# Kernel tuning notes

Hardware: AMD Instinct MI355X
Metric: run time of the kernel (lower is better)

The kernel has to match this reference:

```python
import jax, jax.numpy as jnp
import numpy as np

D_MODEL = 512
D_STATE = 64
SEQ_LEN = 8192
BATCH = 8
LN_EPS = 1e-3  # keras LayerNormalization default epsilon
DELTA_MIN = 0.001
DELTA_MAX = 0.8 * (2.0 / D_STATE)  # default when use_hippo_init=True


def setup_inputs() -> dict:
    key = jax.random.key(0)
    ks = jax.random.split(key, 10)
    x = jax.random.normal(ks[0], (BATCH, SEQ_LEN, D_MODEL), dtype=jnp.float32)
    # Dense layers: glorot-uniform-ish init via scaled normal for simplicity
    def dense_w(k, fan_in, fan_out):
        lim = np.sqrt(6.0 / (fan_in + fan_out))
        return jax.random.uniform(k, (fan_in, fan_out), minval=-lim, maxval=lim, dtype=jnp.float32)
    W_in = dense_w(ks[1], D_MODEL, D_MODEL)
    b_in = jnp.zeros((D_MODEL,), jnp.float32)
    W_xs = dense_w(ks[2], D_MODEL, D_STATE)
    # HiPPO-LegS log init: A_log = log(n+1)
    A_log = jnp.log(jnp.arange(1, D_STATE + 1, dtype=jnp.float32))
    log_delta = jax.random.uniform(ks[3], (D_STATE,), minval=np.log(DELTA_MIN), maxval=np.log(DELTA_MAX), dtype=jnp.float32)
    B = jnp.ones((D_STATE,), jnp.float32)
    C = jax.random.normal(ks[4], (D_STATE,), dtype=jnp.float32)  # stddev=1.0
    D = jnp.ones((D_MODEL,), jnp.float32)
    W_so = dense_w(ks[5], D_STATE, D_MODEL)
    W_out = dense_w(ks[6], D_MODEL, D_MODEL)
    b_out = jnp.zeros((D_MODEL,), jnp.float32)
    ln_gamma = jnp.ones((D_MODEL,), jnp.float32)
    ln_beta = jnp.zeros((D_MODEL,), jnp.float32)
    return {
        "x": x, "ln_gamma": ln_gamma, "ln_beta": ln_beta,
        "W_in": W_in, "b_in": b_in, "W_xs": W_xs,
        "A_log": A_log, "log_delta": log_delta, "B": B, "C": C, "D": D,
        "W_so": W_so, "W_out": W_out, "b_out": b_out,
    }


def reference(x, ln_gamma, ln_beta, W_in, b_in, W_xs, A_log, log_delta, B, C, D, W_so, W_out, b_out):
    Bsz, L, dm = x.shape
    n_fft = 1 << int(np.ceil(np.log2(2 * L - 1)))
    residual = x
    # LayerNorm over last axis (keras default)
    mu = jnp.mean(x, axis=-1, keepdims=True)
    var = jnp.mean(jnp.square(x - mu), axis=-1, keepdims=True)
    xn = (x - mu) * jax.lax.rsqrt(var + LN_EPS) * ln_gamma + ln_beta
    z = xn @ W_in + b_in                       # (B, L, d_model)
    x_state = z @ W_xs                          # (B, L, d_state)
    # Diagonal SSM discretization (bilinear/Tustin)
    A = -jnp.exp(A_log)
    delta = jax.nn.softplus(log_delta)
    dA2 = delta * A / 2.0
    A_bar = (1.0 + dA2) / (1.0 - dA2)           # (d_state,)
    B_bar = delta / (1.0 - dA2) * B             # (d_state,)
    t = jnp.arange(L, dtype=jnp.float32)
    kernel = jnp.power(A_bar[None, :], t[:, None]) * B_bar[None, :]  # (L, d_state)
    # FFT convolution along time
    u_t = jnp.transpose(x_state, (0, 2, 1))     # (B, d_state, L)
    k_t = kernel.T                              # (d_state, L)
    u_f = jnp.fft.rfft(u_t, n=n_fft, axis=-1)
    k_f = jnp.fft.rfft(k_t, n=n_fft, axis=-1)
    y = jnp.fft.irfft(u_f * k_f[None, :, :], n=n_fft, axis=-1)[:, :, :L]
    y_state = jnp.transpose(y, (0, 2, 1))       # (B, L, d_state)
    y_state = y_state * C[None, None, :]
    y = y_state @ W_so                          # (B, L, d_model)
    y = y + D * z
    y = y @ W_out + b_out
    return y + residual
```

## Files before the change

### kernel.cpp

```cpp
#include <hip/hip_runtime.h>
#include <hip/hip_bf16.h>
#include <cstddef>
#include <cstdint>

#define DM 512
#define DS 64
#define L_SEQ 8192
#define NB 8
#define M_ROWS (NB * L_SEQ)
#define LN_EPS 1e-3f
#define NCHUNK 256
#define LCH 32

typedef __attribute__((ext_vector_type(8))) short short8;
typedef __attribute__((ext_vector_type(4))) float f32x4;
using bf16 = __hip_bfloat16;
using ushort_t = unsigned short;

__device__ __forceinline__ unsigned short f2bf(float f) {
    bf16 h = __float2bfloat16(f);
    return *reinterpret_cast<unsigned short*>(&h);
}

__device__ __forceinline__ int swzcol(int row, int col) {
    return (col & ~63) | (((((col >> 3) & 7) ^ (row & 7))) << 3) | (col & 7);
}

__device__ __forceinline__ size_t pkidx(int k, int n, int Kd32) {
    int n16 = n >> 4, fr = n & 15, kt = k >> 5, fq = (k >> 3) & 3, e = k & 7;
    return (((size_t)(n16 * Kd32 + kt) * 64 + fq * 16 + fr) << 3) + e;
}

__device__ __forceinline__ void gload_lds16(const void* g, void* l) {
    __builtin_amdgcn_global_load_lds(
        (const __attribute__((address_space(1))) void*)g,
        (__attribute__((address_space(3))) void*)l, 16, 0, 0);
}

template<int N> __device__ __forceinline__ void wait_vm() {
    static_assert(N == 0 || N == 2, "");
    if constexpr (N == 0) asm volatile("s_waitcnt vmcnt(0)" ::: "memory");
    else                  asm volatile("s_waitcnt vmcnt(2)" ::: "memory");
}

__device__ __forceinline__ void block_barrier() {
    asm volatile("" ::: "memory");
    __builtin_amdgcn_s_barrier();
    asm volatile("" ::: "memory");
}

__global__ __launch_bounds__(256) void prep(const float* __restrict__ W_so,
                                            const float* __restrict__ W_out,
                                            const float* __restrict__ W_in,
                                            const float* __restrict__ W_xs,
                                            const float* __restrict__ b_in,
                                            const float* __restrict__ b_out,
                                            const float* __restrict__ Dv,
                                            float* __restrict__ sWc2,
                                            float* __restrict__ sWc1,
                                            float* __restrict__ bc1,
                                            float* __restrict__ sWc3,
                                            float* __restrict__ bc2)
{
    int i = blockIdx.x * 256 + threadIdx.x;
    if (i < 32768) {
        int s = i >> 9, j = i & 511;
        float a = 0.f;
        for (int c = 0; c < 512; ++c) a += W_so[s * 512 + c] * W_out[c * 512 + j];
        sWc2[i] = a;
    } else if (i < 65536) {
        int idx = i - 32768; int k = idx >> 6, n = idx & 63;
        float a = 0.f;
        for (int c = 0; c < 512; ++c) a += W_in[k * 512 + c] * W_xs[c * 64 + n];
        sWc1[idx] = a;
    } else if (i < 65600) {
        int n = i - 65536;
        float a = 0.f;
        for (int c = 0; c < 512; ++c) a += b_in[c] * W_xs[c * 64 + n];
        bc1[n] = a;
    } else if (i < 327744) {
        int idx = i - 65600; int k = idx >> 9, j = idx & 511;
        float a = 0.f;
        for (int c = 0; c < 512; ++c) a += W_in[k * 512 + c] * Dv[c] * W_out[c * 512 + j];
        sWc3[idx] = a;
    } else if (i < 328256) {
        int j = i - 327744;
        float a = b_out[j];
        for (int c = 0; c < 512; ++c) a += b_in[c] * Dv[c] * W_out[c * 512 + j];
        bc2[j] = a;
    }
}

__global__ __launch_bounds__(256) void pack_all(const float* __restrict__ sWc3,
                                                const float* __restrict__ sWc1,
                                                const float* __restrict__ sWc2,
                                                ushort_t* __restrict__ Wc3Pk,
                                                ushort_t* __restrict__ Wc1Pk,
                                                ushort_t* __restrict__ Wc2Pk)
{
    int i = blockIdx.x * 256 + threadIdx.x;
    if (i < 262144) {
        int k = i >> 9, n = i & 511;
        Wc3Pk[pkidx(k, n, 16)] = f2bf(sWc3[i]);
    } else if (i < 294912) {
        int j = i - 262144; int k = j >> 6, n = j & 63;
        Wc1Pk[pkidx(k, n, 16)] = f2bf(sWc1[j]);
    } else if (i < 327680) {
        int j = i - 294912; int s = j >> 9, n = j & 511;
        Wc2Pk[pkidx(s, n, 2)] = f2bf(sWc2[j]);
    }
}

__global__ __launch_bounds__(64) void ln_kernel(const float* __restrict__ x,
                                                const float* __restrict__ gamma,
                                                const float* __restrict__ beta,
                                                ushort_t* __restrict__ xn)
{
    size_t row = blockIdx.x;
    int lane = threadIdx.x;
    const float4* xr = (const float4*)(x + row * DM);
    float4 v0 = xr[lane * 2];
    float4 v1 = xr[lane * 2 + 1];
    float s  = v0.x + v0.y + v0.z + v0.w + v1.x + v1.y + v1.z + v1.w;
    float s2 = v0.x*v0.x + v0.y*v0.y + v0.z*v0.z + v0.w*v0.w
             + v1.x*v1.x + v1.y*v1.y + v1.z*v1.z + v1.w*v1.w;
    #pragma unroll
    for (int off = 32; off > 0; off >>= 1) {
        s  += __shfl_xor(s,  off);
        s2 += __shfl_xor(s2, off);
    }
    float mu  = s * (1.0f / DM);
    float var = s2 * (1.0f / DM) - mu * mu;
    float rs  = rsqrtf(var + LN_EPS);
    const float4* g4 = (const float4*)gamma;
    const float4* b4 = (const float4*)beta;
    float4 g0 = g4[lane * 2], g1 = g4[lane * 2 + 1];
    float4 bb0 = b4[lane * 2], bb1 = b4[lane * 2 + 1];
    short8 o;
    o[0] = (short)f2bf((v0.x - mu) * rs * g0.x + bb0.x);
    o[1] = (short)f2bf((v0.y - mu) * rs * g0.y + bb0.y);
    o[2] = (short)f2bf((v0.z - mu) * rs * g0.z + bb0.z);
    o[3] = (short)f2bf((v0.w - mu) * rs * g0.w + bb0.w);
    o[4] = (short)f2bf((v1.x - mu) * rs * g1.x + bb1.x);
    o[5] = (short)f2bf((v1.y - mu) * rs * g1.y + bb1.y);
    o[6] = (short)f2bf((v1.z - mu) * rs * g1.z + bb1.z);
    o[7] = (short)f2bf((v1.w - mu) * rs * g1.w + bb1.w);
    int g = (lane & 7) ^ ((int)row & 7);
    *(short8*)(xn + row * DM + (lane >> 3) * 64 + g * 8) = o;
}

__device__ __forceinline__ void store_out(float* C, size_t i, float v) { C[i] = v; }
__device__ __forceinline__ void store_out(bf16* C, size_t i, float v)  { C[i] = __float2bfloat16(v); }

template<int BN, int WR, int WC, typename OutT, bool DUAL, bool HB, bool HA, bool SWZO>
__global__ __launch_bounds__(512, 4) void gemm_bp(const ushort_t* __restrict__ A1,
                                                  const ushort_t* __restrict__ B1,
                                                  const ushort_t* __restrict__ A2,
                                                  const ushort_t* __restrict__ B2,
                                                  const float* __restrict__ bias,
                                                  const float* __restrict__ aux,
                                                  OutT* __restrict__ C,
                                                  int M, int N, int K2)
{
    constexpr int BM = 128;
    constexpr int MF = BM / (16 * WR), NF = BN / (16 * WC);
    static_assert(NF == 2, "b ping-pong arrays assume NF==2");
    __shared__ unsigned char LDS[3][BM * 128];

    const int tid = threadIdx.x;
    const int lane = tid & 63, w = tid >> 6;
    const int fr = lane & 15, fq = lane >> 4;
    const int wr = w % WR, wc = w / WR;

    const int ny = N / BN;
    const int per = (int)gridDim.x >> 3;
    const int lg = ((int)blockIdx.x & 7) * per + ((int)blockIdx.x >> 3);
    const size_t bm0 = (size_t)(lg / ny) * BM;
    const int bn0 = (lg % ny) * BN;
    const int nk = (DUAL ? 1 : 0) + K2 / 64;

    f32x4 acc[MF][NF];
    #pragma unroll
    for (int m = 0; m < MF; ++m)
        #pragma unroll
        for (int n = 0; n < NF; ++n)
            acc[m][n] = (f32x4){0.f, 0.f, 0.f, 0.f};

    auto stage = [&](int buf, int t) {
        #pragma unroll
        for (int j = 0; j < 2; ++j) {
            int r = j * 64 + (tid >> 3);
            const ushort_t* src;
            if constexpr (DUAL) {
                if (t == 0) src = A1 + (bm0 + r) * (size_t)64 + (tid & 7) * 8;
                else        src = A2 + (bm0 + r) * (size_t)512 + (size_t)(t - 1) * 64 + (tid & 7) * 8;
            } else {
                src = A2 + (bm0 + r) * (size_t)K2 + (size_t)t * 64 + (tid & 7) * 8;
            }
            gload_lds16(src, &LDS[buf][j * 8192 + w * 1024]);
        }
    };

    auto loadB = [&](short8 (&bb)[2][2], int t) {
        #pragma unroll
        for (int h = 0; h < 2; ++h)
            #pragma unroll
            for (int n = 0; n < NF; ++n) {
                int n16g = (bn0 + wc * (BN / WC) + n * 16) >> 4;
                const ushort_t* p;
                if constexpr (DUAL) {
                    if (t == 0) p = B1 + (((size_t)(n16g * 2 + h) * 64 + lane) << 3);
                    else        p = B2 + (((size_t)(n16g * 16 + (t - 1) * 2 + h) * 64 + lane) << 3);
                } else {
                    p = B2 + (((size_t)(n16g * (K2 / 32) + t * 2 + h) * 64 + lane) << 3);
                }
                bb[h][n] = *(const short8*)p;
            }
    };

    auto compute = [&](int buf, const short8 (&bb)[2][2]) {
        #pragma unroll
        for (int h = 0; h < 2; ++h) {
            short8 af[MF];
            #pragma unroll
            for (int m = 0; m < MF; ++m) {
                int row = wr * (BM / WR) + m * 16 + fr;
                int g = (h * 4 + fq) ^ (row & 7);
                af[m] = *(const short8*)&LDS[buf][row * 128 + g * 16];
            }
            #pragma unroll
            for (int m = 0; m < MF; ++m)
                #pragma unroll
                for (int n = 0; n < NF; ++n)
                    acc[m][n] = __builtin_amdgcn_mfma_f32_16x16x32_bf16(af[m], bb[h][n], acc[m][n], 0, 0, 0);
        }
    };

    short8 bX[2][2], bY[2][2];
    stage(0, 0);
    loadB(bX, 0);
    if (nk > 1) stage(1, 1);

    #define PHASE(T, BCUR, BNEXT)                                            \
        do {                                                                 \
            if ((T) + 1 < nk) wait_vm<2>(); else wait_vm<0>();               \
            block_barrier();                                                 \
            if ((T) + 1 < nk) loadB(BNEXT, (T) + 1);                         \
            if ((T) + 2 < nk) stage(((T) + 2) % 3, (T) + 2);                 \
            __builtin_amdgcn_sched_barrier(0);                               \
            compute((T) % 3, BCUR);                                          \
        } while (0)

    for (int t = 0; t < nk; t += 2) {
        PHASE(t, bX, bY);
        if (t + 1 < nk) PHASE(t + 1, bY, bX);
    }
    #undef PHASE

    #pragma unroll
    for (int n = 0; n < NF; ++n) {
        int coll = wc * (BN / WC) + n * 16 + fr;
        int colg = bn0 + coll;
        float bv = HB ? bias[colg] : 0.f;
        #pragma unroll
        for (int m = 0; m < MF; ++m) {
            int rowl = wr * (BM / WR) + m * 16 + fq * 4;
            #pragma unroll
            for (int r = 0; r < 4; ++r) {
                size_t row = bm0 + rowl + r;
                float v = acc[m][n][r] + bv;
                if constexpr (HA) v += aux[row * (size_t)N + colg];
                size_t oc = SWZO ? (size_t)swzcol(rowl + r, colg) : (size_t)colg;
                store_out(C, row * (size_t)N + oc, v);
            }
        }
    }
}

__device__ __forceinline__ void ssm_params(const float* A_log, const float* log_delta,
                                           const float* Bv, int n, float& Ab, float& Bb)
{
    float A  = -expf(A_log[n]);
    float dl = log1pf(expf(log_delta[n]));
    float dA2 = dl * A * 0.5f;
    float inv = 1.0f / (1.0f - dA2);
    Ab = (1.0f + dA2) * inv;
    Bb = dl * inv * Bv[n];
}

__global__ __launch_bounds__(64) void scan_pass1(const float* __restrict__ xs,
                                                 const float* __restrict__ A_log,
                                                 const float* __restrict__ log_delta,
                                                 const float* __restrict__ Bv,
                                                 float* __restrict__ carry)
{
    int b = blockIdx.x / NCHUNK;
    int c = blockIdx.x % NCHUNK;
    int n = threadIdx.x;
    float Ab, Bb;
    ssm_params(A_log, log_delta, Bv, n, Ab, Bb);
    size_t base = ((size_t)b * L_SEQ + (size_t)c * LCH) * DS + n;
    float h = 0.0f;
    for (int t = 0; t < LCH; ++t)
        h = Ab * h + Bb * xs[base + (size_t)t * DS];
    carry[((size_t)b * NCHUNK + c) * DS + n] = h;
}

__global__ __launch_bounds__(64) void scan_pass2(const float* __restrict__ A_log,
                                                 const float* __restrict__ log_delta,
                                                 const float* __restrict__ Bv,
                                                 const float* __restrict__ carry,
                                                 float* __restrict__ hin)
{
    int b = blockIdx.x;
    int n = threadIdx.x;
    float Ab, Bb;
    ssm_params(A_log, log_delta, Bv, n, Ab, Bb);
    float powA = powf(Ab, (float)LCH);
    float h = 0.0f;
    for (int c = 0; c < NCHUNK; ++c) {
        size_t idx = ((size_t)b * NCHUNK + c) * DS + n;
        hin[idx] = h;
        h = powA * h + carry[idx];
    }
}

__global__ __launch_bounds__(64) void scan_pass3(const float* __restrict__ xs,
                                                 const float* __restrict__ A_log,
                                                 const float* __restrict__ log_delta,
                                                 const float* __restrict__ Bv,
                                                 const float* __restrict__ Cv,
                                                 const float* __restrict__ hin,
                                                 ushort_t* __restrict__ ys)
{
    int b = blockIdx.x / NCHUNK;
    int c = blockIdx.x % NCHUNK;
    int n = threadIdx.x;
    float Ab, Bb;
    ssm_params(A_log, log_delta, Bv, n, Ab, Bb);
    float Cn = Cv[n];
    size_t base = ((size_t)b * L_SEQ + (size_t)c * LCH) * DS + n;
    size_t rowbase = ((size_t)b * L_SEQ + (size_t)c * LCH) * DS;
    float h = hin[((size_t)b * NCHUNK + c) * DS + n];
    for (int t = 0; t < LCH; ++t) {
        h = Ab * h + Bb * xs[base + (size_t)t * DS];
        int col = (((n >> 3) ^ (t & 7)) << 3) | (n & 7);
        ys[rowbase + (size_t)t * DS + col] = f2bf(Cn * h);
    }
}

extern "C" void kernel_launch(void* const* d_in, const int* in_sizes, int n_in,
                              void* d_out, int out_size, void* d_ws, size_t ws_size,
                              hipStream_t stream)
{
    const float* x         = (const float*)d_in[0];
    const float* ln_gamma  = (const float*)d_in[1];
    const float* ln_beta   = (const float*)d_in[2];
    const float* W_in      = (const float*)d_in[3];
    const float* b_in      = (const float*)d_in[4];
    const float* W_xs      = (const float*)d_in[5];
    const float* A_log     = (const float*)d_in[6];
    const float* log_delta = (const float*)d_in[7];
    const float* Bv        = (const float*)d_in[8];
    const float* Cv        = (const float*)d_in[9];
    const float* Dv        = (const float*)d_in[10];
    const float* W_so      = (const float*)d_in[11];
    const float* W_out     = (const float*)d_in[12];
    const float* b_out     = (const float*)d_in[13];
    float* out = (float*)d_out;

    const size_t M = M_ROWS;
    float*    xs_f   = (float*)d_ws;
    ushort_t* xn_b   = (ushort_t*)(xs_f + M * DS);
    ushort_t* ys_b   = xn_b + M * (size_t)DM;
    ushort_t* Wc3Pk  = ys_b + M * (size_t)DS;
    ushort_t* Wc1Pk  = Wc3Pk + (size_t)DM * DM;
    ushort_t* Wc2Pk  = Wc1Pk + (size_t)DM * DS;
    float*    sWc2   = (float*)(Wc2Pk + (size_t)DS * DM);
    float*    sWc1   = sWc2 + (size_t)DS * DM;
    float*    bc1    = sWc1 + (size_t)DM * DS;
    float*    sWc3   = bc1 + 64;
    float*    bc2    = sWc3 + (size_t)DM * DM;
    float*    carry  = bc2 + DM;
    float*    hin    = carry + NB * NCHUNK * DS;

    prep<<<dim3(1283), dim3(256), 0, stream>>>(W_so, W_out, W_in, W_xs, b_in, b_out, Dv,
                                               sWc2, sWc1, bc1, sWc3, bc2);
    pack_all<<<dim3(1280), dim3(256), 0, stream>>>(sWc3, sWc1, sWc2, Wc3Pk, Wc1Pk, Wc2Pk);
    ln_kernel<<<dim3((unsigned)M), dim3(64), 0, stream>>>(x, ln_gamma, ln_beta, xn_b);
    gemm_bp<64, 4, 2, float, false, true, false, false>
        <<<dim3(M / 128), dim3(512), 0, stream>>>(nullptr, nullptr, xn_b, Wc1Pk,
                                                  bc1, nullptr, xs_f, (int)M, DS, DM);
    scan_pass1<<<dim3(NB * NCHUNK), dim3(64), 0, stream>>>(xs_f, A_log, log_delta, Bv, carry);
    scan_pass2<<<dim3(NB), dim3(64), 0, stream>>>(A_log, log_delta, Bv, carry, hin);
    scan_pass3<<<dim3(NB * NCHUNK), dim3(64), 0, stream>>>(xs_f, A_log, log_delta, Bv, Cv, hin, ys_b);
    gemm_bp<128, 2, 4, float, true, true, true, false>
        <<<dim3((M / 128) * (DM / 128)), dim3(512), 0, stream>>>(ys_b, Wc2Pk, xn_b, Wc3Pk,
                                                                 bc2, x, out, (int)M, DM, DM);
}
```

Before: 212.5 us.

## Pre-pack activations into MFMA fragment layout and stream GEMM operands from global

LayerNorm and scan outputs are now written directly in the MFMA fragment-packed layout, so both GEMMs can load A and B fragments straight from global memory into registers with double buffering, without LDS staging or barriers. The LDS-based block-tiled GEMM is replaced by a per-wave streaming kernel in which each wave owns a 32xN tile. This removes LDS traffic and synchronisation, but it loses cross-wave reuse of A through LDS, and B fragments are re-read by every wave, which raises global/L2 traffic.

Measured after the change: 309.4 us. 45.6% more time.

```diff
diff --git a/kernel.cpp b/kernel.cpp
--- a/kernel.cpp
+++ b/kernel.cpp
@@ -22,31 +22,9 @@
     return *reinterpret_cast<unsigned short*>(&h);
 }
 
-__device__ __forceinline__ int swzcol(int row, int col) {
-    return (col & ~63) | (((((col >> 3) & 7) ^ (row & 7))) << 3) | (col & 7);
-}
-
-__device__ __forceinline__ size_t pkidx(int k, int n, int Kd32) {
-    int n16 = n >> 4, fr = n & 15, kt = k >> 5, fq = (k >> 3) & 3, e = k & 7;
-    return (((size_t)(n16 * Kd32 + kt) * 64 + fq * 16 + fr) << 3) + e;
-}
-
-__device__ __forceinline__ void gload_lds16(const void* g, void* l) {
-    __builtin_amdgcn_global_load_lds(
-        (const __attribute__((address_space(1))) void*)g,
-        (__attribute__((address_space(3))) void*)l, 16, 0, 0);
-}
-
-template<int N> __device__ __forceinline__ void wait_vm() {
-    static_assert(N == 0 || N == 2, "");
-    if constexpr (N == 0) asm volatile("s_waitcnt vmcnt(0)" ::: "memory");
-    else                  asm volatile("s_waitcnt vmcnt(2)" ::: "memory");
-}
-
-__device__ __forceinline__ void block_barrier() {
-    asm volatile("" ::: "memory");
-    __builtin_amdgcn_s_barrier();
-    asm volatile("" ::: "memory");
+__device__ __forceinline__ size_t pkidx(int k, int idx, int Kd32) {
+    int i16 = idx >> 4, fr = idx & 15, kt = k >> 5, fq = (k >> 3) & 3, e = k & 7;
+    return (((size_t)(i16 * Kd32 + kt) * 64 + fq * 16 + fr) << 3) + e;
 }
 
 __global__ __launch_bounds__(256) void prep(const float* __restrict__ W_so,
@@ -145,133 +123,88 @@
     o[5] = (short)f2bf((v1.y - mu) * rs * g1.y + bb1.y);
     o[6] = (short)f2bf((v1.z - mu) * rs * g1.z + bb1.z);
     o[7] = (short)f2bf((v1.w - mu) * rs * g1.w + bb1.w);
-    int g = (lane & 7) ^ ((int)row & 7);
-    *(short8*)(xn + row * DM + (lane >> 3) * 64 + g * 8) = o;
-}
-
-__device__ __forceinline__ void store_out(float* C, size_t i, float v) { C[i] = v; }
-__device__ __forceinline__ void store_out(bf16* C, size_t i, float v)  { C[i] = __float2bfloat16(v); }
-
-template<int BN, int WR, int WC, typename OutT, bool DUAL, bool HB, bool HA, bool SWZO>
-__global__ __launch_bounds__(512, 4) void gemm_bp(const ushort_t* __restrict__ A1,
-                                                  const ushort_t* __restrict__ B1,
-                                                  const ushort_t* __restrict__ A2,
-                                                  const ushort_t* __restrict__ B2,
-                                                  const float* __restrict__ bias,
-                                                  const float* __restrict__ aux,
-                                                  OutT* __restrict__ C,
-                                                  int M, int N, int K2)
-{
-    constexpr int BM = 128;
-    constexpr int MF = BM / (16 * WR), NF = BN / (16 * WC);
-    static_assert(NF == 2, "b ping-pong arrays assume NF==2");
-    __shared__ unsigned char LDS[3][BM * 128];
-
+    *(short8*)(xn + pkidx(lane * 8, (int)row, 16)) = o;
+}
+
+template<int NS1, int NS2, int CTS, bool HB, bool HA>
+__global__ __launch_bounds__(512) void gemm_stream(const ushort_t* __restrict__ A1,
+                                                   const ushort_t* __restrict__ B1,
+                                                   const ushort_t* __restrict__ A2,
+                                                   const ushort_t* __restrict__ B2,
+                                                   const float* __restrict__ bias,
+                                                   const float* __restrict__ aux,
+                                                   float* __restrict__ C,
+                                                   int N)
+{
+    constexpr int NS = NS1 + NS2;
     const int tid = threadIdx.x;
     const int lane = tid & 63, w = tid >> 6;
     const int fr = lane & 15, fq = lane >> 4;
-    const int wr = w % WR, wc = w / WR;
-
-    const int ny = N / BN;
+
     const int per = (int)gridDim.x >> 3;
     const int lg = ((int)blockIdx.x & 7) * per + ((int)blockIdx.x >> 3);
-    const size_t bm0 = (size_t)(lg / ny) * BM;
-    const int bn0 = (lg % ny) * BN;
-    const int nk = (DUAL ? 1 : 0) + K2 / 64;
-
-    f32x4 acc[MF][NF];
+    const int ct = w % CTS;
+    const int rt = lg * (8 / CTS) + w / CTS;
+    const int m16g = rt * 2;
+    const int n16g = ct * 4;
+
+    f32x4 acc[2][4];
     #pragma unroll
-    for (int m = 0; m < MF; ++m)
+    for (int m = 0; m < 2; ++m)
         #pragma unroll
-        for (int n = 0; n < NF; ++n)
+        for (int n = 0; n < 4; ++n)
             acc[m][n] = (f32x4){0.f, 0.f, 0.f, 0.f};
 
-    auto stage = [&](int buf, int t) {
+    short8 a[2][2], b[2][4];
+
+    #define ISSUE(BUF, S)                                                         \
+        do {                                                                      \
+            constexpr int kt_ = ((S) < NS1) ? (S) : ((S) - NS1);                  \
+            constexpr int Kd_ = ((S) < NS1) ? NS1 : NS2;                          \
+            const ushort_t* Ab_ = ((S) < NS1) ? A1 : A2;                          \
+            const ushort_t* Bb_ = ((S) < NS1) ? B1 : B2;                          \
+            _Pragma("unroll")                                                     \
+            for (int m = 0; m < 2; ++m)                                           \
+                a[BUF][m] = *(const short8*)(Ab_ +                                \
+                    ((((size_t)(m16g + m) * Kd_ + kt_) * 64 + lane) << 3));       \
+            _Pragma("unroll")                                                     \
+            for (int n = 0; n < 4; ++n)                                           \
+                b[BUF][n] = *(const short8*)(Bb_ +                                \
+                    ((((size_t)(n16g + n) * Kd_ + kt_) * 64 + lane) << 3));       \
+        } while (0)
+
+    ISSUE(0, 0);
+    #pragma unroll
+    for (int s = 0; s < NS; ++s) {
+        if (s + 1 < NS) {
+            switch (s + 1) {
+                #define CASE(SS) case SS: if constexpr (SS < NS) ISSUE((SS) & 1, SS); break;
+                CASE(1) CASE(2) CASE(3) CASE(4) CASE(5) CASE(6) CASE(7) CASE(8) CASE(9)
+                CASE(10) CASE(11) CASE(12) CASE(13) CASE(14) CASE(15) CASE(16) CASE(17)
+                #undef CASE
+            }
+        }
         #pragma unroll
-        for (int j = 0; j < 2; ++j) {
-            int r = j * 64 + (tid >> 3);
-            const ushort_t* src;
-            if constexpr (DUAL) {
-                if (t == 0) src = A1 + (bm0 + r) * (size_t)64 + (tid & 7) * 8;
-                else        src = A2 + (bm0 + r) * (size_t)512 + (size_t)(t - 1) * 64 + (tid & 7) * 8;
-            } else {
-                src = A2 + (bm0 + r) * (size_t)K2 + (size_t)t * 64 + (tid & 7) * 8;
-            }
-            gload_lds16(src, &LDS[buf][j * 8192 + w * 1024]);
-        }
-    };
-
-    auto loadB = [&](short8 (&bb)[2][2], int t) {
-        #pragma unroll
-        for (int h = 0; h < 2; ++h)
+        for (int m = 0; m < 2; ++m)
             #pragma unroll
-            for (int n = 0; n < NF; ++n) {
-                int n16g = (bn0 + wc * (BN / WC) + n * 16) >> 4;
-                const ushort_t* p;
-                if constexpr (DUAL) {
-                    if (t == 0) p = B1 + (((size_t)(n16g * 2 + h) * 64 + lane) << 3);
-                    else        p = B2 + (((size_t)(n16g * 16 + (t - 1) * 2 + h) * 64 + lane) << 3);
-                } else {
-                    p = B2 + (((size_t)(n16g * (K2 / 32) + t * 2 + h) * 64 + lane) << 3);
-                }
-                bb[h][n] = *(const short8*)p;
-            }
-    };
-
-    auto compute = [&](int buf, const short8 (&bb)[2][2]) {
-        #pragma unroll
-        for (int h = 0; h < 2; ++h) {
-            short8 af[MF];
-            #pragma unroll
-            for (int m = 0; m < MF; ++m) {
-                int row = wr * (BM / WR) + m * 16 + fr;
-                int g = (h * 4 + fq) ^ (row & 7);
-                af[m] = *(const short8*)&LDS[buf][row * 128 + g * 16];
-            }
-            #pragma unroll
-            for (int m = 0; m < MF; ++m)
-                #pragma unroll
-                for (int n = 0; n < NF; ++n)
-                    acc[m][n] = __builtin_amdgcn_mfma_f32_16x16x32_bf16(af[m], bb[h][n], acc[m][n], 0, 0, 0);
-        }
-    };
-
-    short8 bX[2][2], bY[2][2];
-    stage(0, 0);
-    loadB(bX, 0);
-    if (nk > 1) stage(1, 1);
-
-    #define PHASE(T, BCUR, BNEXT)                                            \
-        do {                                                                 \
-            if ((T) + 1 < nk) wait_vm<2>(); else wait_vm<0>();               \
-            block_barrier();                                                 \
-            if ((T) + 1 < nk) loadB(BNEXT, (T) + 1);                         \
-            if ((T) + 2 < nk) stage(((T) + 2) % 3, (T) + 2);                 \
-            __builtin_amdgcn_sched_barrier(0);                               \
-            compute((T) % 3, BCUR);                                          \
-        } while (0)
-
-    for (int t = 0; t < nk; t += 2) {
-        PHASE(t, bX, bY);
-        if (t + 1 < nk) PHASE(t + 1, bY, bX);
-    }
-    #undef PHASE
+            for (int n = 0; n < 4; ++n)
+                acc[m][n] = __builtin_amdgcn_mfma_f32_16x16x32_bf16(a[s & 1][m], b[s & 1][n], acc[m][n], 0, 0, 0);
+    }
+    #undef ISSUE
 
     #pragma unroll
-    for (int n = 0; n < NF; ++n) {
-        int coll = wc * (BN / WC) + n * 16 + fr;
-        int colg = bn0 + coll;
+    for (int n = 0; n < 4; ++n) {
+        int colg = (n16g + n) * 16 + fr;
         float bv = HB ? bias[colg] : 0.f;
         #pragma unroll
-        for (int m = 0; m < MF; ++m) {
-            int rowl = wr * (BM / WR) + m * 16 + fq * 4;
+        for (int m = 0; m < 2; ++m) {
+            size_t row0 = (size_t)(m16g + m) * 16 + fq * 4;
             #pragma unroll
             for (int r = 0; r < 4; ++r) {
-                size_t row = bm0 + rowl + r;
+                size_t idx = (row0 + r) * (size_t)N + colg;
                 float v = acc[m][n][r] + bv;
-                if constexpr (HA) v += aux[row * (size_t)N + colg];
-                size_t oc = SWZO ? (size_t)swzcol(rowl + r, colg) : (size_t)colg;
-                store_out(C, row * (size_t)N + oc, v);
+                if constexpr (HA) v += aux[idx];
+                C[idx] = v;
             }
         }
     }
@@ -340,12 +273,11 @@
     ssm_params(A_log, log_delta, Bv, n, Ab, Bb);
     float Cn = Cv[n];
     size_t base = ((size_t)b * L_SEQ + (size_t)c * LCH) * DS + n;
-    size_t rowbase = ((size_t)b * L_SEQ + (size_t)c * LCH) * DS;
+    int grow0 = b * L_SEQ + c * LCH;
     float h = hin[((size_t)b * NCHUNK + c) * DS + n];
     for (int t = 0; t < LCH; ++t) {
         h = Ab * h + Bb * xs[base + (size_t)t * DS];
-        int col = (((n >> 3) ^ (t & 7)) << 3) | (n & 7);
-        ys[rowbase + (size_t)t * DS + col] = f2bf(Cn * h);
+        ys[pkidx(n, grow0 + t, 2)] = f2bf(Cn * h);
     }
 }
 
@@ -371,9 +303,9 @@
 
     const size_t M = M_ROWS;
     float*    xs_f   = (float*)d_ws;
-    ushort_t* xn_b   = (ushort_t*)(xs_f + M * DS);
-    ushort_t* ys_b   = xn_b + M * (size_t)DM;
-    ushort_t* Wc3Pk  = ys_b + M * (size_t)DS;
+    ushort_t* xn_pk  = (ushort_t*)(xs_f + M * DS);
+    ushort_t* ys_pk  = xn_pk + M * (size_t)DM;
+    ushort_t* Wc3Pk  = ys_pk + M * (size_t)DS;
     ushort_t* Wc1Pk  = Wc3Pk + (size_t)DM * DM;
     ushort_t* Wc2Pk  = Wc1Pk + (size_t)DM * DS;
     float*    sWc2   = (float*)(Wc2Pk + (size_t)DS * DM);
@@ -387,14 +319,14 @@
     prep<<<dim3(1283), dim3(256), 0, stream>>>(W_so, W_out, W_in, W_xs, b_in, b_out, Dv,
                                                sWc2, sWc1, bc1, sWc3, bc2);
     pack_all<<<dim3(1280), dim3(256), 0, stream>>>(sWc3, sWc1, sWc2, Wc3Pk, Wc1Pk, Wc2Pk);
-    ln_kernel<<<dim3((unsigned)M), dim3(64), 0, stream>>>(x, ln_gamma, ln_beta, xn_b);
-    gemm_bp<64, 4, 2, float, false, true, false, false>
-        <<<dim3(M / 128), dim3(512), 0, stream>>>(nullptr, nullptr, xn_b, Wc1Pk,
-                                                  bc1, nullptr, xs_f, (int)M, DS, DM);
+    ln_kernel<<<dim3((unsigned)M), dim3(64), 0, stream>>>(x, ln_gamma, ln_beta, xn_pk);
+    gemm_stream<0, 16, 1, true, false>
+        <<<dim3(M / 256), dim3(512), 0, stream>>>(nullptr, nullptr, xn_pk, Wc1Pk,
+                                                  bc1, nullptr, xs_f, DS);
     scan_pass1<<<dim3(NB * NCHUNK), dim3(64), 0, stream>>>(xs_f, A_log, log_delta, Bv, carry);
     scan_pass2<<<dim3(NB), dim3(64), 0, stream>>>(A_log, log_delta, Bv, carry, hin);
-    scan_pass3<<<dim3(NB * NCHUNK), dim3(64), 0, stream>>>(xs_f, A_log, log_delta, Bv, Cv, hin, ys_b);
-    gemm_bp<128, 2, 4, float, true, true, true, false>
-        <<<dim3((M / 128) * (DM / 128)), dim3(512), 0, stream>>>(ys_b, Wc2Pk, xn_b, Wc3Pk,
-                                                                 bc2, x, out, (int)M, DM, DM);
-}
+    scan_pass3<<<dim3(NB * NCHUNK), dim3(64), 0, stream>>>(xs_f, A_log, log_delta, Bv, Cv, hin, ys_pk);
+    gemm_stream<2, 16, 8, true, true>
+        <<<dim3(M / 32), dim3(512), 0, stream>>>(ys_pk, Wc2Pk, xn_pk, Wc3Pk,
+                                                 bc2, x, out, DM);
+}
```

## Fuse LayerNorm with the x_state projection GEMM via LDS-staged MFMA

Applied to the files above, without the earlier changes.

Replaces the separate LayerNorm kernel and the skinny 512->64 GEMM with one kernel. Each block normalizes 16 rows, writes them to global memory and to LDS, then four waves each compute a 16-column slice of x_state with bf16 MFMA from the packed weights. This removes re-reading the normalized activations from global memory and one kernel launch. In exchange, weight fragments are read from global memory without LDS reuse across the many small blocks, and the LDS tile per block may limit occupancy.

After: 214.1 us. Within noise of the previous version (+0.8%).

```diff
diff --git a/kernel.cpp b/kernel.cpp
--- a/kernel.cpp
+++ b/kernel.cpp
@@ -111,42 +111,70 @@
     }
 }
 
-__global__ __launch_bounds__(64) void ln_kernel(const float* __restrict__ x,
-                                                const float* __restrict__ gamma,
-                                                const float* __restrict__ beta,
-                                                ushort_t* __restrict__ xn)
-{
-    size_t row = blockIdx.x;
-    int lane = threadIdx.x;
-    const float4* xr = (const float4*)(x + row * DM);
-    float4 v0 = xr[lane * 2];
-    float4 v1 = xr[lane * 2 + 1];
-    float s  = v0.x + v0.y + v0.z + v0.w + v1.x + v1.y + v1.z + v1.w;
-    float s2 = v0.x*v0.x + v0.y*v0.y + v0.z*v0.z + v0.w*v0.w
-             + v1.x*v1.x + v1.y*v1.y + v1.z*v1.z + v1.w*v1.w;
-    #pragma unroll
-    for (int off = 32; off > 0; off >>= 1) {
-        s  += __shfl_xor(s,  off);
-        s2 += __shfl_xor(s2, off);
-    }
-    float mu  = s * (1.0f / DM);
-    float var = s2 * (1.0f / DM) - mu * mu;
-    float rs  = rsqrtf(var + LN_EPS);
+__global__ __launch_bounds__(256) void ln_xs(const float* __restrict__ x,
+                                             const float* __restrict__ gamma,
+                                             const float* __restrict__ beta,
+                                             const ushort_t* __restrict__ Wc1Pk,
+                                             const float* __restrict__ bc1,
+                                             ushort_t* __restrict__ xn,
+                                             float* __restrict__ xs)
+{
+    __shared__ ushort_t xt[16 * 512];
+    const int tid = threadIdx.x;
+    const int lane = tid & 63, w = tid >> 6;
+    const int fr = lane & 15, fq = lane >> 4;
+    const size_t row0 = (size_t)blockIdx.x * 16;
+
     const float4* g4 = (const float4*)gamma;
     const float4* b4 = (const float4*)beta;
     float4 g0 = g4[lane * 2], g1 = g4[lane * 2 + 1];
     float4 bb0 = b4[lane * 2], bb1 = b4[lane * 2 + 1];
-    short8 o;
-    o[0] = (short)f2bf((v0.x - mu) * rs * g0.x + bb0.x);
-    o[1] = (short)f2bf((v0.y - mu) * rs * g0.y + bb0.y);
-    o[2] = (short)f2bf((v0.z - mu) * rs * g0.z + bb0.z);
-    o[3] = (short)f2bf((v0.w - mu) * rs * g0.w + bb0.w);
-    o[4] = (short)f2bf((v1.x - mu) * rs * g1.x + bb1.x);
-    o[5] = (short)f2bf((v1.y - mu) * rs * g1.y + bb1.y);
-    o[6] = (short)f2bf((v1.z - mu) * rs * g1.z + bb1.z);
-    o[7] = (short)f2bf((v1.w - mu) * rs * g1.w + bb1.w);
-    int g = (lane & 7) ^ ((int)row & 7);
-    *(short8*)(xn + row * DM + (lane >> 3) * 64 + g * 8) = o;
+
+    #pragma unroll
+    for (int rr = 0; rr < 4; ++rr) {
+        int r = w * 4 + rr;
+        size_t row = row0 + r;
+        const float4* xr = (const float4*)(x + row * DM);
+        float4 v0 = xr[lane * 2], v1 = xr[lane * 2 + 1];
+        float s  = v0.x + v0.y + v0.z + v0.w + v1.x + v1.y + v1.z + v1.w;
+        float s2 = v0.x*v0.x + v0.y*v0.y + v0.z*v0.z + v0.w*v0.w
+                 + v1.x*v1.x + v1.y*v1.y + v1.z*v1.z + v1.w*v1.w;
+        #pragma unroll
+        for (int off = 32; off > 0; off >>= 1) {
+            s  += __shfl_xor(s,  off);
+            s2 += __shfl_xor(s2, off);
+        }
+        float mu  = s * (1.0f / DM);
+        float var = s2 * (1.0f / DM) - mu * mu;
+        float rs  = rsqrtf(var + LN_EPS);
+        short8 o;
+        o[0] = (short)f2bf((v0.x - mu) * rs * g0.x + bb0.x);
+        o[1] = (short)f2bf((v0.y - mu) * rs * g0.y + bb0.y);
+        o[2] = (short)f2bf((v0.z - mu) * rs * g0.z + bb0.z);
+        o[3] = (short)f2bf((v0.w - mu) * rs * g0.w + bb0.w);
+        o[4] = (short)f2bf((v1.x - mu) * rs * g1.x + bb1.x);
+        o[5] = (short)f2bf((v1.y - mu) * rs * g1.y + bb1.y);
+        o[6] = (short)f2bf((v1.z - mu) * rs * g1.z + bb1.z);
+        o[7] = (short)f2bf((v1.w - mu) * rs * g1.w + bb1.w);
+        int g = (lane & 7) ^ ((int)row & 7);
+        *(short8*)(xn + row * DM + (lane >> 3) * 64 + g * 8) = o;
+        *(short8*)&xt[r * 512 + (lane >> 3) * 64 + g * 8] = o;
+    }
+    __syncthreads();
+
+    f32x4 acc = (f32x4){0.f, 0.f, 0.f, 0.f};
+    #pragma unroll
+    for (int kt = 0; kt < 16; ++kt) {
+        int seg = kt >> 1;
+        int gk = ((kt & 1) * 4 + fq) ^ (fr & 7);
+        short8 af = *(const short8*)&xt[fr * 512 + seg * 64 + gk * 8];
+        short8 bf = *(const short8*)(Wc1Pk + (((size_t)(w * 16 + kt) * 64 + lane) << 3));
+        acc = __builtin_amdgcn_mfma_f32_16x16x32_bf16(af, bf, acc, 0, 0, 0);
+    }
+    float bv = bc1[w * 16 + fr];
+    #pragma unroll
+    for (int r2 = 0; r2 < 4; ++r2)
+        xs[(row0 + fq * 4 + r2) * DS + w * 16 + fr] = acc[r2] + bv;
 }
 
 __device__ __forceinline__ void store_out(float* C, size_t i, float v) { C[i] = v; }
@@ -387,10 +415,8 @@
     prep<<<dim3(1283), dim3(256), 0, stream>>>(W_so, W_out, W_in, W_xs, b_in, b_out, Dv,
                                                sWc2, sWc1, bc1, sWc3, bc2);
     pack_all<<<dim3(1280), dim3(256), 0, stream>>>(sWc3, sWc1, sWc2, Wc3Pk, Wc1Pk, Wc2Pk);
-    ln_kernel<<<dim3((unsigned)M), dim3(64), 0, stream>>>(x, ln_gamma, ln_beta, xn_b);
-    gemm_bp<64, 4, 2, float, false, true, false, false>
-        <<<dim3(M / 128), dim3(512), 0, stream>>>(nullptr, nullptr, xn_b, Wc1Pk,
-                                                  bc1, nullptr, xs_f, (int)M, DS, DM);
+    ln_xs<<<dim3((unsigned)(M / 16)), dim3(256), 0, stream>>>(x, ln_gamma, ln_beta,
+                                                              Wc1Pk, bc1, xn_b, xs_f);
     scan_pass1<<<dim3(NB * NCHUNK), dim3(64), 0, stream>>>(xs_f, A_log, log_delta, Bv, carry);
     scan_pass2<<<dim3(NB), dim3(64), 0, stream>>>(A_log, log_delta, Bv, carry, hin);
     scan_pass3<<<dim3(NB * NCHUNK), dim3(64), 0, stream>>>(xs_f, A_log, log_delta, Bv, Cv, hin, ys_b);
```
